# Kernel optimization log

Hardware: AMD Instinct MI355X
Metric: run time of the kernel (lower is better)

The kernel has to match this reference:

```python
import jax, jax.numpy as jnp
import numpy as np

TEMPERATURE = 0.5
EPS = 1e-8  # F.cosine_similarity default eps
NEG_FILL = -1e9  # fill_diagonal_(-1000000000.0)


def setup_inputs() -> dict:
    key = jax.random.key(0)
    k1, k2 = jax.random.split(key)
    N, D = 4096, 256
    zi = jax.random.normal(k1, (N, D), dtype=jnp.float32)
    zj = jax.random.normal(k2, (N, D), dtype=jnp.float32)
    return {"zi": zi, "zj": zj}


def reference(zi, zj):
    N = zi.shape[0]
    z = jnp.concatenate([zi, zj], axis=0)  # [2N, D]
    # cosine similarity: normalize once, then a single GEMM
    norms = jnp.sqrt(jnp.sum(z * z, axis=1, keepdims=True))
    zn = z / jnp.maximum(norms, EPS)
    sim = jnp.matmul(zn, zn.T) / TEMPERATURE  # [2N, 2N]
    idx = jnp.arange(2 * N)
    sim = sim.at[idx, idx].set(NEG_FILL)  # mask self-similarity
    labels = jnp.concatenate([jnp.arange(N) + N, jnp.arange(N)])
    # CrossEntropyLoss(reduction='sum'): sum_i (logsumexp(row_i) - row_i[label_i])
    logp = jax.nn.log_softmax(sim, axis=1)
    loss = -jnp.sum(logp[idx, labels])
    return loss / (2 * N)
```

## Files before the change

### kernel.cpp

```cpp
#include <hip/hip_runtime.h>
#include <hip/hip_bf16.h>
#include <math.h>


using short8  = __attribute__((ext_vector_type(8))) short;
using floatx4 = __attribute__((ext_vector_type(4))) float;

constexpr int TWO_N = 8192;
constexpr int DIM   = 256;
constexpr int NB    = 64;
constexpr int NTRI  = NB * (NB + 1) / 2;
constexpr float INV2N = 1.0f / 8192.0f;

__device__ static inline unsigned short f2bf(float f) {
  unsigned u = __float_as_uint(f);
  return (unsigned short)((u + 0x7fffu + ((u >> 16) & 1u)) >> 16);
}

__device__ static inline void async_copy16(const __hip_bfloat16* g, __hip_bfloat16* l) {
  __builtin_amdgcn_global_load_lds(
      (const __attribute__((address_space(1))) void*)(const void*)g,
      (__attribute__((address_space(3))) void*)(void*)l, 16, 0, 0);
}

__global__ __launch_bounds__(256) void k_normalize(
    const float* __restrict__ zi, const float* __restrict__ zj,
    __hip_bfloat16* __restrict__ zn, float* __restrict__ rowtotal,
    float* __restrict__ out)
{
  if (blockIdx.x == 0 && threadIdx.x == 0) out[0] = 0.0f;
  if (blockIdx.x < 32) rowtotal[blockIdx.x * 256 + threadIdx.x] = 0.0f;

  const int lane = threadIdx.x & 63;
  const int wave = threadIdx.x >> 6;
  const int row  = blockIdx.x * 4 + wave;
  const float* src = (row < 4096) ? (zi + (size_t)row * DIM)
                                  : (zj + (size_t)(row - 4096) * DIM);
  float4 v = reinterpret_cast<const float4*>(src)[lane];
  float ss = v.x * v.x + v.y * v.y + v.z * v.z + v.w * v.w;
#pragma unroll
  for (int m = 32; m >= 1; m >>= 1) ss += __shfl_xor(ss, m, 64);
  float inv = 1.0f / fmaxf(sqrtf(ss), 1e-8f);
  ushort4 o;
  o.x = f2bf(v.x * inv); o.y = f2bf(v.y * inv);
  o.z = f2bf(v.z * inv); o.w = f2bf(v.w * inv);
  reinterpret_cast<ushort4*>(zn + (size_t)row * DIM)[lane] = o;
}

__global__ __launch_bounds__(256) void k_simexp(
    const __hip_bfloat16* __restrict__ Z, float* __restrict__ rowtotal,
    float* __restrict__ out)
{
  __shared__ __align__(16) char smem[128 * 64 * 2 * 2];
  __shared__ float colsum[128];
  __hip_bfloat16* As = (__hip_bfloat16*)smem;
  __hip_bfloat16* Bs = As + 128 * 64;
  float* scratch = (float*)smem;

  const int tid  = threadIdx.x;
  const int lane = tid & 63;
  const int wave = tid >> 6;
  const int wm   = wave >> 1;
  const int wn   = wave & 1;

  const int bid = blockIdx.x;
  const int u   = (bid & 7) * (NTRI / 8) + (bid >> 3);

  int jb = (int)((sqrtf(8.0f * (float)u + 1.0f) - 1.0f) * 0.5f);
  while ((jb + 1) * (jb + 2) / 2 <= u) ++jb;
  while (jb * (jb + 1) / 2 > u) --jb;
  const int ib = u - jb * (jb + 1) / 2;

  const bool diagblk = (ib == jb);
  const bool pairblk = (jb == ib + 32);
  const int i0 = ib * 128;
  const int j0 = jb * 128;

  if (tid < 128) colsum[tid] = 0.0f;

  floatx4 acc[4][4] = {};

  const int lane7 = lane & 7;
  const int sub   = lane >> 3;
  const int gkoff = ((lane7 ^ sub) << 3);
  const int q     = lane >> 4;
  const int c16   = lane & 15;

  const __hip_bfloat16* gbase =
      Z + (size_t)((wave < 2 ? i0 : j0) + (wave & 1) * 64) * DIM;
  __hip_bfloat16* lbase = ((wave < 2) ? As : Bs) + (wave & 1) * 64 * 64;

  for (int kk = 0; kk < 4; ++kk) {
    const int k0 = kk * 64;
#pragma unroll
    for (int c = 0; c < 8; ++c) {
      const __hip_bfloat16* gp = gbase + (size_t)(c * 8 + sub) * DIM + k0 + gkoff;
      async_copy16(gp, lbase + c * 512);
    }
    __syncthreads();

#pragma unroll
    for (int ks = 0; ks < 2; ++ks) {
      const int phys = (ks * 4 + q) ^ lane7;
      short8 a[4], b[4];
#pragma unroll
      for (int mt = 0; mt < 4; ++mt)
        a[mt] = *reinterpret_cast<const short8*>(
            As + (wm * 64 + mt * 16 + c16) * 64 + phys * 8);
#pragma unroll
      for (int nt = 0; nt < 4; ++nt)
        b[nt] = *reinterpret_cast<const short8*>(
            Bs + (wn * 64 + nt * 16 + c16) * 64 + phys * 8);
#pragma unroll
      for (int mt = 0; mt < 4; ++mt)
#pragma unroll
        for (int nt = 0; nt < 4; ++nt)
          acc[mt][nt] = __builtin_amdgcn_mfma_f32_16x16x32_bf16(
              a[mt], b[nt], acc[mt][nt], 0, 0, 0);
    }
    __syncthreads();
  }

  float colacc[4] = {0.f, 0.f, 0.f, 0.f};
  float rowacc[4][4];
  float pc = 0.f;
  const bool diagwave = (wm == wn);

#pragma unroll
  for (int mt = 0; mt < 4; ++mt) {
#pragma unroll
    for (int reg = 0; reg < 4; ++reg) {
      const bool onquad = (c16 == q * 4 + reg);
      float s = 0.0f;
#pragma unroll
      for (int nt = 0; nt < 4; ++nt) {
        float e = __expf(2.0f * acc[mt][nt][reg] - 2.0f);
        bool skip = diagblk && diagwave && (nt == mt) && onquad;
        s += skip ? 0.0f : e;
        colacc[nt] += e;
      }
      if (pairblk && diagwave && onquad) pc += acc[mt][mt][reg];
      rowacc[mt][reg] = s;
    }
  }

  if (!diagblk) {
#pragma unroll
    for (int nt = 0; nt < 4; ++nt) {
      float cs = colacc[nt];
      cs += __shfl_xor(cs, 16, 64);
      cs += __shfl_xor(cs, 32, 64);
      if (lane < 16) atomicAdd(&colsum[wn * 64 + nt * 16 + lane], cs);
    }
  }

  if (pairblk && diagwave) {
#pragma unroll
    for (int m = 32; m >= 1; m >>= 1) pc += __shfl_xor(pc, m, 64);
    if (lane == 0) atomicAdd(out, -4.0f * pc * INV2N);
  }

#pragma unroll
  for (int mt = 0; mt < 4; ++mt)
#pragma unroll
    for (int reg = 0; reg < 4; ++reg)
      scratch[(wm * 64 + mt * 16 + q * 4 + reg) * 33 + wn * 16 + c16] =
          rowacc[mt][reg];

  __syncthreads();

  if (tid < 128) {
    float rs = 0.0f;
#pragma unroll
    for (int k = 0; k < 32; ++k) rs += scratch[tid * 33 + k];
    atomicAdd(&rowtotal[i0 + tid], rs);
    if (!diagblk) atomicAdd(&rowtotal[j0 + tid], colsum[tid]);
  }
}

__global__ __launch_bounds__(256) void k_finalize(
    const float* __restrict__ rowtotal, float* __restrict__ out)
{
  __shared__ float wsum[4];
  const int lane = threadIdx.x & 63;
  const int wave = threadIdx.x >> 6;
  const int row  = blockIdx.x * 256 + threadIdx.x;
  float v = 2.0f + __logf(rowtotal[row]);
#pragma unroll
  for (int m = 32; m >= 1; m >>= 1) v += __shfl_xor(v, m, 64);
  if (lane == 0) wsum[wave] = v;
  __syncthreads();
  if (threadIdx.x == 0)
    atomicAdd(out, (wsum[0] + wsum[1] + wsum[2] + wsum[3]) * INV2N);
}

extern "C" void kernel_launch(void* const* d_in, const int* in_sizes, int n_in,
                              void* d_out, int out_size, void* d_ws, size_t ws_size,
                              hipStream_t stream) {
  const float* zi = (const float*)d_in[0];
  const float* zj = (const float*)d_in[1];
  float* out = (float*)d_out;

  __hip_bfloat16* zn = (__hip_bfloat16*)d_ws;
  float* rowtotal = (float*)((char*)d_ws + (size_t)TWO_N * DIM * 2);

  k_normalize<<<dim3(TWO_N / 4), dim3(256), 0, stream>>>(zi, zj, zn, rowtotal, out);
  k_simexp<<<dim3(NTRI), dim3(256), 0, stream>>>(zn, rowtotal, out);
  k_finalize<<<dim3(TWO_N / 256), dim3(256), 0, stream>>>(rowtotal, out);
}
```

Measured before the change: 90.16 us.

## Fuse finalize into simexp via ticket, use 8-wave blocks, persistent normalize

Removes the separate finalize launch by having the last simexp block, chosen with an atomic ticket counter, compute the logsumexp reduction. The simexp block grows from 4 to 8 waves with a 2x4 wave grid, so each wave holds half the accumulators, which should raise occupancy and latency hiding. The row-sum scratch now uses a stride-64 layout read with a rotated index. The normalize kernel now runs 128 blocks that each process 16 rows per wave with software-prefetched loads, cutting block count. Costs include a tail where one block does all 8192 log ops serially, plus the ordering risk in the last-block pattern.

```diff
diff --git a/kernel.cpp b/kernel.cpp
--- a/kernel.cpp
+++ b/kernel.cpp
@@ -26,33 +26,44 @@
 __global__ __launch_bounds__(256) void k_normalize(
     const float* __restrict__ zi, const float* __restrict__ zj,
     __hip_bfloat16* __restrict__ zn, float* __restrict__ rowtotal,
-    float* __restrict__ out)
+    float* __restrict__ out, unsigned* __restrict__ ticket)
 {
-  if (blockIdx.x == 0 && threadIdx.x == 0) out[0] = 0.0f;
+  if (blockIdx.x == 0 && threadIdx.x == 0) { out[0] = 0.0f; ticket[0] = 0u; }
   if (blockIdx.x < 32) rowtotal[blockIdx.x * 256 + threadIdx.x] = 0.0f;
 
   const int lane = threadIdx.x & 63;
   const int wave = threadIdx.x >> 6;
-  const int row  = blockIdx.x * 4 + wave;
-  const float* src = (row < 4096) ? (zi + (size_t)row * DIM)
-                                  : (zj + (size_t)(row - 4096) * DIM);
-  float4 v = reinterpret_cast<const float4*>(src)[lane];
-  float ss = v.x * v.x + v.y * v.y + v.z * v.z + v.w * v.w;
-#pragma unroll
-  for (int m = 32; m >= 1; m >>= 1) ss += __shfl_xor(ss, m, 64);
-  float inv = 1.0f / fmaxf(sqrtf(ss), 1e-8f);
-  ushort4 o;
-  o.x = f2bf(v.x * inv); o.y = f2bf(v.y * inv);
-  o.z = f2bf(v.z * inv); o.w = f2bf(v.w * inv);
-  reinterpret_cast<ushort4*>(zn + (size_t)row * DIM)[lane] = o;
-}
-
-__global__ __launch_bounds__(256) void k_simexp(
+  const int gw   = blockIdx.x * 4 + wave;
+
+  auto srcptr = [&](int it) -> const float* {
+    return ((it < 8) ? zi : zj) + (size_t)(gw + (it & 7) * 512) * DIM;
+  };
+
+  float4 v = reinterpret_cast<const float4*>(srcptr(0))[lane];
+#pragma unroll
+  for (int it = 0; it < 16; ++it) {
+    float4 vn;
+    if (it < 15) vn = reinterpret_cast<const float4*>(srcptr(it + 1))[lane];
+    float ss = v.x * v.x + v.y * v.y + v.z * v.z + v.w * v.w;
+#pragma unroll
+    for (int m = 32; m >= 1; m >>= 1) ss += __shfl_xor(ss, m, 64);
+    float inv = 1.0f / fmaxf(sqrtf(ss), 1e-8f);
+    ushort4 o;
+    o.x = f2bf(v.x * inv); o.y = f2bf(v.y * inv);
+    o.z = f2bf(v.z * inv); o.w = f2bf(v.w * inv);
+    reinterpret_cast<ushort4*>(zn + (size_t)(gw + it * 512) * DIM)[lane] = o;
+    v = vn;
+  }
+}
+
+__global__ __launch_bounds__(512) void k_simexp(
     const __hip_bfloat16* __restrict__ Z, float* __restrict__ rowtotal,
-    float* __restrict__ out)
+    float* __restrict__ out, unsigned* __restrict__ ticket)
 {
   __shared__ __align__(16) char smem[128 * 64 * 2 * 2];
   __shared__ float colsum[128];
+  __shared__ float finsum[8];
+  __shared__ int lastflag;
   __hip_bfloat16* As = (__hip_bfloat16*)smem;
   __hip_bfloat16* Bs = As + 128 * 64;
   float* scratch = (float*)smem;
@@ -60,8 +71,8 @@
   const int tid  = threadIdx.x;
   const int lane = tid & 63;
   const int wave = tid >> 6;
-  const int wm   = wave >> 1;
-  const int wn   = wave & 1;
+  const int wm   = wave >> 2;
+  const int wn   = wave & 3;
 
   const int bid = blockIdx.x;
   const int u   = (bid & 7) * (NTRI / 8) + (bid >> 3);
@@ -78,7 +89,7 @@
 
   if (tid < 128) colsum[tid] = 0.0f;
 
-  floatx4 acc[4][4] = {};
+  floatx4 acc[4][2] = {};
 
   const int lane7 = lane & 7;
   const int sub   = lane >> 3;
@@ -87,13 +98,13 @@
   const int c16   = lane & 15;
 
   const __hip_bfloat16* gbase =
-      Z + (size_t)((wave < 2 ? i0 : j0) + (wave & 1) * 64) * DIM;
-  __hip_bfloat16* lbase = ((wave < 2) ? As : Bs) + (wave & 1) * 64 * 64;
+      Z + (size_t)((wave < 4 ? i0 : j0) + (wave & 3) * 32) * DIM;
+  __hip_bfloat16* lbase = ((wave < 4) ? As : Bs) + (wave & 3) * 32 * 64;
 
   for (int kk = 0; kk < 4; ++kk) {
     const int k0 = kk * 64;
 #pragma unroll
-    for (int c = 0; c < 8; ++c) {
+    for (int c = 0; c < 4; ++c) {
       const __hip_bfloat16* gp = gbase + (size_t)(c * 8 + sub) * DIM + k0 + gkoff;
       async_copy16(gp, lbase + c * 512);
     }
@@ -102,59 +113,61 @@
 #pragma unroll
     for (int ks = 0; ks < 2; ++ks) {
       const int phys = (ks * 4 + q) ^ lane7;
-      short8 a[4], b[4];
+      short8 a[4], b[2];
 #pragma unroll
       for (int mt = 0; mt < 4; ++mt)
         a[mt] = *reinterpret_cast<const short8*>(
             As + (wm * 64 + mt * 16 + c16) * 64 + phys * 8);
 #pragma unroll
-      for (int nt = 0; nt < 4; ++nt)
+      for (int nt = 0; nt < 2; ++nt)
         b[nt] = *reinterpret_cast<const short8*>(
-            Bs + (wn * 64 + nt * 16 + c16) * 64 + phys * 8);
+            Bs + (wn * 32 + nt * 16 + c16) * 64 + phys * 8);
 #pragma unroll
       for (int mt = 0; mt < 4; ++mt)
 #pragma unroll
-        for (int nt = 0; nt < 4; ++nt)
+        for (int nt = 0; nt < 2; ++nt)
           acc[mt][nt] = __builtin_amdgcn_mfma_f32_16x16x32_bf16(
               a[mt], b[nt], acc[mt][nt], 0, 0, 0);
     }
     __syncthreads();
   }
 
-  float colacc[4] = {0.f, 0.f, 0.f, 0.f};
+  const bool diagw = ((wn >> 1) == wm);
+  const int  h     = wn & 1;
+  float colacc[2] = {0.f, 0.f};
   float rowacc[4][4];
   float pc = 0.f;
-  const bool diagwave = (wm == wn);
 
 #pragma unroll
   for (int mt = 0; mt < 4; ++mt) {
 #pragma unroll
     for (int reg = 0; reg < 4; ++reg) {
       const bool onquad = (c16 == q * 4 + reg);
+      const bool mdiag  = diagw && onquad && ((mt >> 1) == h);
       float s = 0.0f;
 #pragma unroll
-      for (int nt = 0; nt < 4; ++nt) {
+      for (int nt = 0; nt < 2; ++nt) {
         float e = __expf(2.0f * acc[mt][nt][reg] - 2.0f);
-        bool skip = diagblk && diagwave && (nt == mt) && onquad;
+        bool skip = diagblk && mdiag && (nt == (mt & 1));
         s += skip ? 0.0f : e;
         colacc[nt] += e;
       }
-      if (pairblk && diagwave && onquad) pc += acc[mt][mt][reg];
+      if (pairblk && mdiag) pc += acc[mt][mt & 1][reg];
       rowacc[mt][reg] = s;
     }
   }
 
   if (!diagblk) {
 #pragma unroll
-    for (int nt = 0; nt < 4; ++nt) {
+    for (int nt = 0; nt < 2; ++nt) {
       float cs = colacc[nt];
       cs += __shfl_xor(cs, 16, 64);
       cs += __shfl_xor(cs, 32, 64);
-      if (lane < 16) atomicAdd(&colsum[wn * 64 + nt * 16 + lane], cs);
-    }
-  }
-
-  if (pairblk && diagwave) {
+      if (lane < 16) atomicAdd(&colsum[wn * 32 + nt * 16 + lane], cs);
+    }
+  }
+
+  if (pairblk && diagw) {
 #pragma unroll
     for (int m = 32; m >= 1; m >>= 1) pc += __shfl_xor(pc, m, 64);
     if (lane == 0) atomicAdd(out, -4.0f * pc * INV2N);
@@ -164,7 +177,7 @@
   for (int mt = 0; mt < 4; ++mt)
 #pragma unroll
     for (int reg = 0; reg < 4; ++reg)
-      scratch[(wm * 64 + mt * 16 + q * 4 + reg) * 33 + wn * 16 + c16] =
+      scratch[(wm * 64 + mt * 16 + q * 4 + reg) * 64 + wn * 16 + c16] =
           rowacc[mt][reg];
 
   __syncthreads();
@@ -172,26 +185,35 @@
   if (tid < 128) {
     float rs = 0.0f;
 #pragma unroll
-    for (int k = 0; k < 32; ++k) rs += scratch[tid * 33 + k];
+    for (int k = 0; k < 64; ++k)
+      rs += scratch[tid * 64 + ((k + tid) & 63)];
     atomicAdd(&rowtotal[i0 + tid], rs);
     if (!diagblk) atomicAdd(&rowtotal[j0 + tid], colsum[tid]);
   }
-}
-
-__global__ __launch_bounds__(256) void k_finalize(
-    const float* __restrict__ rowtotal, float* __restrict__ out)
-{
-  __shared__ float wsum[4];
-  const int lane = threadIdx.x & 63;
-  const int wave = threadIdx.x >> 6;
-  const int row  = blockIdx.x * 256 + threadIdx.x;
-  float v = 2.0f + __logf(rowtotal[row]);
-#pragma unroll
-  for (int m = 32; m >= 1; m >>= 1) v += __shfl_xor(v, m, 64);
-  if (lane == 0) wsum[wave] = v;
+
   __syncthreads();
-  if (threadIdx.x == 0)
-    atomicAdd(out, (wsum[0] + wsum[1] + wsum[2] + wsum[3]) * INV2N);
+  if (tid == 0) lastflag = (atomicAdd(ticket, 1u) == (unsigned)(NTRI - 1)) ? 1 : 0;
+  __syncthreads();
+  if (lastflag) {
+    __threadfence();
+    float v = 0.0f;
+#pragma unroll 4
+    for (int r = tid; r < TWO_N; r += 512) {
+      float tv = __hip_atomic_load(&rowtotal[r], __ATOMIC_RELAXED,
+                                   __HIP_MEMORY_SCOPE_AGENT);
+      v += 2.0f + __logf(tv);
+    }
+#pragma unroll
+    for (int m = 32; m >= 1; m >>= 1) v += __shfl_xor(v, m, 64);
+    if (lane == 0) finsum[wave] = v;
+    __syncthreads();
+    if (tid == 0) {
+      float acc8 = 0.0f;
+#pragma unroll
+      for (int w = 0; w < 8; ++w) acc8 += finsum[w];
+      atomicAdd(out, acc8 * INV2N);
+    }
+  }
 }
 
 extern "C" void kernel_launch(void* const* d_in, const int* in_sizes, int n_in,
@@ -203,8 +225,8 @@
 
   __hip_bfloat16* zn = (__hip_bfloat16*)d_ws;
   float* rowtotal = (float*)((char*)d_ws + (size_t)TWO_N * DIM * 2);
-
-  k_normalize<<<dim3(TWO_N / 4), dim3(256), 0, stream>>>(zi, zj, zn, rowtotal, out);
-  k_simexp<<<dim3(NTRI), dim3(256), 0, stream>>>(zn, rowtotal, out);
-  k_finalize<<<dim3(TWO_N / 256), dim3(256), 0, stream>>>(rowtotal, out);
-}
+  unsigned* ticket = (unsigned*)((char*)d_ws + (size_t)TWO_N * DIM * 2 + (size_t)TWO_N * 4);
+
+  k_normalize<<<dim3(128), dim3(256), 0, stream>>>(zi, zj, zn, rowtotal, out, ticket);
+  k_simexp<<<dim3(NTRI), dim3(512), 0, stream>>>(zn, rowtotal, out, ticket);
+}
```

Measured after the change: 108.6 us. +20.4%, slower.

## Fuse finalize into simexp via last-block ticket and shrink normalize grid

Applied to the files above, without the earlier changes.

Removes the separate finalize kernel launch. A global ticket counter lets the last simexp block compute the log-sum over all row totals, using atomic loads after a fence. The normalize kernel now runs 128 blocks, each wave handling 16 rows with a software-prefetched next load, instead of one row per wave. This saves a launch and a kernel boundary. The cost is that one block does the whole serial final reduction over 8192 rows, and fewer normalize blocks may underuse bandwidth.

```diff
diff --git a/kernel.cpp b/kernel.cpp
--- a/kernel.cpp
+++ b/kernel.cpp
@@ -26,33 +26,44 @@
 __global__ __launch_bounds__(256) void k_normalize(
     const float* __restrict__ zi, const float* __restrict__ zj,
     __hip_bfloat16* __restrict__ zn, float* __restrict__ rowtotal,
-    float* __restrict__ out)
+    float* __restrict__ out, unsigned* __restrict__ ticket)
 {
-  if (blockIdx.x == 0 && threadIdx.x == 0) out[0] = 0.0f;
+  if (blockIdx.x == 0 && threadIdx.x == 0) { out[0] = 0.0f; ticket[0] = 0u; }
   if (blockIdx.x < 32) rowtotal[blockIdx.x * 256 + threadIdx.x] = 0.0f;
 
   const int lane = threadIdx.x & 63;
   const int wave = threadIdx.x >> 6;
-  const int row  = blockIdx.x * 4 + wave;
-  const float* src = (row < 4096) ? (zi + (size_t)row * DIM)
-                                  : (zj + (size_t)(row - 4096) * DIM);
-  float4 v = reinterpret_cast<const float4*>(src)[lane];
-  float ss = v.x * v.x + v.y * v.y + v.z * v.z + v.w * v.w;
-#pragma unroll
-  for (int m = 32; m >= 1; m >>= 1) ss += __shfl_xor(ss, m, 64);
-  float inv = 1.0f / fmaxf(sqrtf(ss), 1e-8f);
-  ushort4 o;
-  o.x = f2bf(v.x * inv); o.y = f2bf(v.y * inv);
-  o.z = f2bf(v.z * inv); o.w = f2bf(v.w * inv);
-  reinterpret_cast<ushort4*>(zn + (size_t)row * DIM)[lane] = o;
+  const int gw   = blockIdx.x * 4 + wave;
+
+  auto srcptr = [&](int it) -> const float* {
+    return ((it < 8) ? zi : zj) + (size_t)(gw + (it & 7) * 512) * DIM;
+  };
+
+  float4 v = reinterpret_cast<const float4*>(srcptr(0))[lane];
+#pragma unroll
+  for (int it = 0; it < 16; ++it) {
+    float4 vn;
+    if (it < 15) vn = reinterpret_cast<const float4*>(srcptr(it + 1))[lane];
+    float ss = v.x * v.x + v.y * v.y + v.z * v.z + v.w * v.w;
+#pragma unroll
+    for (int m = 32; m >= 1; m >>= 1) ss += __shfl_xor(ss, m, 64);
+    float inv = 1.0f / fmaxf(sqrtf(ss), 1e-8f);
+    ushort4 o;
+    o.x = f2bf(v.x * inv); o.y = f2bf(v.y * inv);
+    o.z = f2bf(v.z * inv); o.w = f2bf(v.w * inv);
+    reinterpret_cast<ushort4*>(zn + (size_t)(gw + it * 512) * DIM)[lane] = o;
+    v = vn;
+  }
 }
 
 __global__ __launch_bounds__(256) void k_simexp(
     const __hip_bfloat16* __restrict__ Z, float* __restrict__ rowtotal,
-    float* __restrict__ out)
+    float* __restrict__ out, unsigned* __restrict__ ticket)
 {
   __shared__ __align__(16) char smem[128 * 64 * 2 * 2];
   __shared__ float colsum[128];
+  __shared__ float finsum[4];
+  __shared__ int lastflag;
   __hip_bfloat16* As = (__hip_bfloat16*)smem;
   __hip_bfloat16* Bs = As + 128 * 64;
   float* scratch = (float*)smem;
@@ -176,22 +187,26 @@
     atomicAdd(&rowtotal[i0 + tid], rs);
     if (!diagblk) atomicAdd(&rowtotal[j0 + tid], colsum[tid]);
   }
-}
-
-__global__ __launch_bounds__(256) void k_finalize(
-    const float* __restrict__ rowtotal, float* __restrict__ out)
-{
-  __shared__ float wsum[4];
-  const int lane = threadIdx.x & 63;
-  const int wave = threadIdx.x >> 6;
-  const int row  = blockIdx.x * 256 + threadIdx.x;
-  float v = 2.0f + __logf(rowtotal[row]);
-#pragma unroll
-  for (int m = 32; m >= 1; m >>= 1) v += __shfl_xor(v, m, 64);
-  if (lane == 0) wsum[wave] = v;
+
   __syncthreads();
-  if (threadIdx.x == 0)
-    atomicAdd(out, (wsum[0] + wsum[1] + wsum[2] + wsum[3]) * INV2N);
+  if (tid == 0) lastflag = (atomicAdd(ticket, 1u) == (unsigned)(NTRI - 1)) ? 1 : 0;
+  __syncthreads();
+  if (lastflag) {
+    __threadfence();
+    float v = 0.0f;
+#pragma unroll 4
+    for (int r = tid; r < TWO_N; r += 256) {
+      float tv = __hip_atomic_load(&rowtotal[r], __ATOMIC_RELAXED,
+                                   __HIP_MEMORY_SCOPE_AGENT);
+      v += 2.0f + __logf(tv);
+    }
+#pragma unroll
+    for (int m = 32; m >= 1; m >>= 1) v += __shfl_xor(v, m, 64);
+    if (lane == 0) finsum[wave] = v;
+    __syncthreads();
+    if (tid == 0)
+      atomicAdd(out, (finsum[0] + finsum[1] + finsum[2] + finsum[3]) * INV2N);
+  }
 }
 
 extern "C" void kernel_launch(void* const* d_in, const int* in_sizes, int n_in,
@@ -203,8 +218,8 @@
 
   __hip_bfloat16* zn = (__hip_bfloat16*)d_ws;
   float* rowtotal = (float*)((char*)d_ws + (size_t)TWO_N * DIM * 2);
-
-  k_normalize<<<dim3(TWO_N / 4), dim3(256), 0, stream>>>(zi, zj, zn, rowtotal, out);
-  k_simexp<<<dim3(NTRI), dim3(256), 0, stream>>>(zn, rowtotal, out);
-  k_finalize<<<dim3(TWO_N / 256), dim3(256), 0, stream>>>(rowtotal, out);
-}
+  unsigned* ticket = (unsigned*)((char*)d_ws + (size_t)TWO_N * DIM * 2 + (size_t)TWO_N * 4);
+
+  k_normalize<<<dim3(128), dim3(256), 0, stream>>>(zi, zj, zn, rowtotal, out, ticket);
+  k_simexp<<<dim3(NTRI), dim3(256), 0, stream>>>(zn, rowtotal, out, ticket);
+}
```

After: 104.1 us. 1.15x slower.
